# Performance work log

Measured on AMD Instinct MI355X. Metric: run time of the kernel, lower is better.

The kernel has to match this reference:

```python
import jax, jax.numpy as jnp
import numpy as np

TEMPERATURE = 1.0

def setup_inputs() -> dict:
    key = jax.random.key(0)
    k1, k2 = jax.random.split(key)
    B, I, O = 256, 1024, 1024
    x = jax.random.normal(k1, (B, I), dtype=jnp.float32)
    # mimic TruncatedNormal(stddev=1/sqrt(input_size)) init
    w = jax.random.normal(k2, (I, O), dtype=jnp.float32) * (1.0 / np.sqrt(I))
    b = jnp.zeros((O,), dtype=jnp.float32)
    return {"x": x, "w": w, "b": b}

def reference(x, w, b):
    # z: [B, I, O] outer product per sample
    z = jnp.einsum('bi,io->bio', x, w)
    n = x.shape[-1]
    # per-output-neuron temperature softmax over the input dim I
    s = jax.nn.softmax(jnp.abs(z) / TEMPERATURE, axis=1)
    out = n * jnp.sum(z * s, axis=1)  # [B, O]
    return out + b
```

## Files before the change

kernel.cpp:

```cpp
#include <hip/hip_runtime.h>

#define BDIM 256
#define IDIM 1024
#define ODIM 1024

#define TILE_O 64
#define TILE_B 4
#define NW 8
#define QLEN (IDIM / NW)

typedef float v2f __attribute__((ext_vector_type(2)));

#if __has_builtin(__builtin_amdgcn_exp2f)
#define FAST_EXP2(v) __builtin_amdgcn_exp2f(v)
#else
#define FAST_EXP2(v) exp2f(v)
#endif

__global__ __launch_bounds__(512, 8)
void stl_kernel(const float* __restrict__ x,
                const float* __restrict__ w,
                const float* __restrict__ bias,
                float* __restrict__ out) {
  __shared__ float xs[TILE_B][IDIM];
  __shared__ float ps[NW][TILE_O][8];

  const int tx = threadIdx.x;
  const int ty = threadIdx.y;
  const int tid = ty * 64 + tx;
  const int o0 = blockIdx.x * TILE_O;
  const int b0 = blockIdx.y * TILE_B;

  const float LOG2E = 1.4426950408889634f;

#pragma unroll
  for (int k = 0; k < 2; ++k) {
    int f = tid + k * 512;
    int row = f >> 8;
    int col = f & 255;
    float4 v = ((const float4*)(x + (size_t)(b0 + row) * IDIM))[col];
    v.x *= LOG2E; v.y *= LOG2E; v.z *= LOG2E; v.w *= LOG2E;
    ((float4*)(&xs[row][0]))[col] = v;
  }
  __syncthreads();

  const int qbase = ty * QLEN;
  const float* wp = w + (size_t)qbase * ODIM + o0 + tx;

  v2f num01 = {0.0f, 0.0f}, num23 = {0.0f, 0.0f};
  v2f den01 = {0.0f, 0.0f}, den23 = {0.0f, 0.0f};

#pragma unroll 2
  for (int j = 0; j < QLEN; j += 4) {
    float wv[4];
#pragma unroll
    for (int u = 0; u < 4; ++u) wv[u] = wp[(size_t)(j + u) * ODIM];
    float4 xq0 = *(const float4*)(&xs[0][qbase + j]);
    float4 xq1 = *(const float4*)(&xs[1][qbase + j]);
    float4 xq2 = *(const float4*)(&xs[2][qbase + j]);
    float4 xq3 = *(const float4*)(&xs[3][qbase + j]);
    const float x0[4] = {xq0.x, xq0.y, xq0.z, xq0.w};
    const float x1[4] = {xq1.x, xq1.y, xq1.z, xq1.w};
    const float x2[4] = {xq2.x, xq2.y, xq2.z, xq2.w};
    const float x3[4] = {xq3.x, xq3.y, xq3.z, xq3.w};
#pragma unroll
    for (int u = 0; u < 4; ++u) {
      v2f p01 = {x0[u] * wv[u], x1[u] * wv[u]};
      v2f p23 = {x2[u] * wv[u], x3[u] * wv[u]};
      v2f t01, t23;
      t01.x = FAST_EXP2(__builtin_fabsf(p01.x));
      t01.y = FAST_EXP2(__builtin_fabsf(p01.y));
      t23.x = FAST_EXP2(__builtin_fabsf(p23.x));
      t23.y = FAST_EXP2(__builtin_fabsf(p23.y));
      num01 += p01 * t01; den01 += t01;
      num23 += p23 * t23; den23 += t23;
    }
  }

  *(float4*)(&ps[ty][tx][0]) = make_float4(num01.x, num01.y, num23.x, num23.y);
  *(float4*)(&ps[ty][tx][4]) = make_float4(den01.x, den01.y, den23.x, den23.y);
  __syncthreads();

  if (ty == 0) {
    float n[4] = {0, 0, 0, 0}, d[4] = {0, 0, 0, 0};
#pragma unroll
    for (int q = 0; q < NW; ++q) {
      float4 a = *(const float4*)(&ps[q][tx][0]);
      float4 b = *(const float4*)(&ps[q][tx][4]);
      n[0] += a.x; n[1] += a.y; n[2] += a.z; n[3] += a.w;
      d[0] += b.x; d[1] += b.y; d[2] += b.z; d[3] += b.w;
    }
    const float LN2 = 0.6931471805599453f;
    const float scale = (float)IDIM * LN2;
    const int o = o0 + tx;
    const float bo = bias[o];
#pragma unroll
    for (int r = 0; r < 4; ++r)
      out[(size_t)(b0 + r) * ODIM + o] = scale * n[r] / d[r] + bo;
  }
}

extern "C" void kernel_launch(void* const* d_in, const int* in_sizes, int n_in,
                              void* d_out, int out_size, void* d_ws, size_t ws_size,
                              hipStream_t stream) {
  const float* x = (const float*)d_in[0];
  const float* w = (const float*)d_in[1];
  const float* b = (const float*)d_in[2];
  float* out = (float*)d_out;

  dim3 grid(ODIM / TILE_O, BDIM / TILE_B);
  dim3 block(64, NW);
  stl_kernel<<<grid, block, 0, stream>>>(x, w, b, out);
}
```

Measured before the change: 95.14 us.

## Software-pipeline weight loads, drop packed v2f math, and parallelize final reduction

Loads the next 8 rows of weights into registers while computing on the current 8, double-buffering the global loads. The packed v2f arithmetic becomes scalar fma with per-row accumulators. The partial-sum layout is transposed so four waves each reduce one batch row instead of a single wave handling all four. The aim is to hide global load latency and shorten the serial epilogue, at the cost of more registers and one redundant wrapped prefetch on the last iteration.

Result: slower. 99.88 us (+5.0%).

```diff
diff --git a/kernel.cpp b/kernel.cpp
--- a/kernel.cpp
+++ b/kernel.cpp
@@ -8,8 +8,6 @@
 #define TILE_B 4
 #define NW 8
 #define QLEN (IDIM / NW)
-
-typedef float v2f __attribute__((ext_vector_type(2)));
 
 #if __has_builtin(__builtin_amdgcn_exp2f)
 #define FAST_EXP2(v) __builtin_amdgcn_exp2f(v)
@@ -23,7 +21,7 @@
                 const float* __restrict__ bias,
                 float* __restrict__ out) {
   __shared__ float xs[TILE_B][IDIM];
-  __shared__ float ps[NW][TILE_O][8];
+  __shared__ float ps[NW][8][TILE_O];
 
   const int tx = threadIdx.x;
   const int ty = threadIdx.y;
@@ -45,58 +43,60 @@
   __syncthreads();
 
   const int qbase = ty * QLEN;
-  const float* wp = w + (size_t)qbase * ODIM + o0 + tx;
+  const int vidx = o0 + tx;
 
-  v2f num01 = {0.0f, 0.0f}, num23 = {0.0f, 0.0f};
-  v2f den01 = {0.0f, 0.0f}, den23 = {0.0f, 0.0f};
+  float num[TILE_B] = {0, 0, 0, 0};
+  float den[TILE_B] = {0, 0, 0, 0};
 
-#pragma unroll 2
-  for (int j = 0; j < QLEN; j += 4) {
-    float wv[4];
+  float wv[8];
 #pragma unroll
-    for (int u = 0; u < 4; ++u) wv[u] = wp[(size_t)(j + u) * ODIM];
-    float4 xq0 = *(const float4*)(&xs[0][qbase + j]);
-    float4 xq1 = *(const float4*)(&xs[1][qbase + j]);
-    float4 xq2 = *(const float4*)(&xs[2][qbase + j]);
-    float4 xq3 = *(const float4*)(&xs[3][qbase + j]);
-    const float x0[4] = {xq0.x, xq0.y, xq0.z, xq0.w};
-    const float x1[4] = {xq1.x, xq1.y, xq1.z, xq1.w};
-    const float x2[4] = {xq2.x, xq2.y, xq2.z, xq2.w};
-    const float x3[4] = {xq3.x, xq3.y, xq3.z, xq3.w};
+  for (int u = 0; u < 8; ++u)
+    wv[u] = (w + (size_t)(qbase + u) * ODIM)[vidx];
+
+  for (int j = 0; j < QLEN; j += 8) {
+    float wc[8];
 #pragma unroll
-    for (int u = 0; u < 4; ++u) {
-      v2f p01 = {x0[u] * wv[u], x1[u] * wv[u]};
-      v2f p23 = {x2[u] * wv[u], x3[u] * wv[u]};
-      v2f t01, t23;
-      t01.x = FAST_EXP2(__builtin_fabsf(p01.x));
-      t01.y = FAST_EXP2(__builtin_fabsf(p01.y));
-      t23.x = FAST_EXP2(__builtin_fabsf(p23.x));
-      t23.y = FAST_EXP2(__builtin_fabsf(p23.y));
-      num01 += p01 * t01; den01 += t01;
-      num23 += p23 * t23; den23 += t23;
+    for (int u = 0; u < 8; ++u) wc[u] = wv[u];
+    {
+      const int jn = (j + 8) & (QLEN - 1);
+#pragma unroll
+      for (int u = 0; u < 8; ++u)
+        wv[u] = (w + (size_t)(qbase + jn + u) * ODIM)[vidx];
+    }
+
+#pragma unroll
+    for (int r = 0; r < TILE_B; ++r) {
+      float4 x0 = *(const float4*)(&xs[r][qbase + j]);
+      float4 x1 = *(const float4*)(&xs[r][qbase + j + 4]);
+      const float xv[8] = {x0.x, x0.y, x0.z, x0.w, x1.x, x1.y, x1.z, x1.w};
+#pragma unroll
+      for (int u = 0; u < 8; ++u) {
+        float p = xv[u] * wc[u];
+        float t = FAST_EXP2(__builtin_fabsf(p));
+        num[r] = __builtin_fmaf(p, t, num[r]);
+        den[r] += t;
+      }
     }
   }
 
-  *(float4*)(&ps[ty][tx][0]) = make_float4(num01.x, num01.y, num23.x, num23.y);
-  *(float4*)(&ps[ty][tx][4]) = make_float4(den01.x, den01.y, den23.x, den23.y);
+#pragma unroll
+  for (int r = 0; r < TILE_B; ++r) {
+    ps[ty][r][tx] = num[r];
+    ps[ty][4 + r][tx] = den[r];
+  }
   __syncthreads();
 
-  if (ty == 0) {
-    float n[4] = {0, 0, 0, 0}, d[4] = {0, 0, 0, 0};
+  if (ty < TILE_B) {
+    float n = 0.0f, d = 0.0f;
 #pragma unroll
     for (int q = 0; q < NW; ++q) {
-      float4 a = *(const float4*)(&ps[q][tx][0]);
-      float4 b = *(const float4*)(&ps[q][tx][4]);
-      n[0] += a.x; n[1] += a.y; n[2] += a.z; n[3] += a.w;
-      d[0] += b.x; d[1] += b.y; d[2] += b.z; d[3] += b.w;
+      n += ps[q][ty][tx];
+      d += ps[q][4 + ty][tx];
     }
     const float LN2 = 0.6931471805599453f;
     const float scale = (float)IDIM * LN2;
     const int o = o0 + tx;
-    const float bo = bias[o];
-#pragma unroll
-    for (int r = 0; r < 4; ++r)
-      out[(size_t)(b0 + r) * ODIM + o] = scale * n[r] / d[r] + bo;
+    out[(size_t)(b0 + ty) * ODIM + o] = scale * n / d + bias[o];
   }
 }
 
```
